# Optimization experiments

Hardware: AMD Instinct MI355X
Metric: run time of the kernel (lower is better)

## Reference

```python
import jax, jax.numpy as jnp
import numpy as np

N_NODES = 100000
N_EDGES = 3200000
F_IN = 128
NOUT = 32


def _lin(x, W, b):
    return x @ W + b


def _spect_conv(x, src, dst, W, b, n_nodes):
    # edge_attr is all-ones with a single frequency (K=1), so SpectConv reduces to
    # an unweighted scatter-add of linearly transformed source-node features.
    h = x @ W                                   # [N, nout]
    agg = jax.ops.segment_sum(h[src], dst, num_segments=n_nodes)  # [N, nout]
    return agg + b


def setup_inputs() -> dict:
    key = jax.random.key(0)
    ks = jax.random.split(key, 32)
    s = 0.05

    def w(k, shape):
        return jax.random.normal(k, shape, dtype=jnp.float32) * s

    inp = {
        "x": jax.random.normal(ks[0], (N_NODES, F_IN), dtype=jnp.float32),
        "edge_index": jax.random.randint(ks[1], (2, N_EDGES), 0, N_NODES, dtype=jnp.int32),
        # SpectConv weights (single frequency) + biases
        "Wc1": w(ks[2], (F_IN, NOUT)), "bc1": jnp.zeros((NOUT,), jnp.float32),
        "Wc2": w(ks[3], (NOUT, NOUT)), "bc2": jnp.zeros((NOUT,), jnp.float32),
        "Wc3": w(ks[4], (NOUT, NOUT)), "bc3": jnp.zeros((NOUT,), jnp.float32),
        # dense branch weights
        "W11": w(ks[5], (F_IN, NOUT)), "b11": w(ks[6], (NOUT,)),
        "W12": w(ks[7], (F_IN, NOUT)), "b12": w(ks[8], (NOUT,)),
        "W13": w(ks[9], (F_IN, NOUT)), "b13": w(ks[10], (NOUT,)),
        "W21": w(ks[11], (NOUT, NOUT)), "b21": w(ks[12], (NOUT,)),
        "W22": w(ks[13], (NOUT, NOUT)), "b22": w(ks[14], (NOUT,)),
        "W23": w(ks[15], (NOUT, NOUT)), "b23": w(ks[16], (NOUT,)),
        "W31": w(ks[17], (NOUT, NOUT)), "b31": w(ks[18], (NOUT,)),
        "W32": w(ks[19], (NOUT, NOUT)), "b32": w(ks[20], (NOUT,)),
        "W33": w(ks[21], (NOUT, NOUT)), "b33": w(ks[22], (NOUT,)),
        "W2": w(ks[23], (NOUT, 1)), "b2": w(ks[24], (1,)),
    }
    return inp


def reference(x, edge_index,
              Wc1, bc1, Wc2, bc2, Wc3, bc3,
              W11, b11, W12, b12, W13, b13,
              W21, b21, W22, b22, W23, b23,
              W31, b31, W32, b32, W33, b33,
              W2, b2):
    src, dst = edge_index[0], edge_index[1]
    n = x.shape[0]
    relu = jax.nn.relu

    def block(h, Wa, ba, Wc, bc, Wm1, bm1, Wm2, bm2):
        return (relu(_lin(h, Wa, ba))
                + relu(_spect_conv(h, src, dst, Wc, bc, n))
                + relu(_lin(h, Wm1, bm1) * _lin(h, Wm2, bm2)))

    h = block(x, W11, b11, Wc1, bc1, W12, b12, W13, b13)
    h = block(h, W21, b21, Wc2, bc2, W22, b22, W23, b23)
    h = block(h, W31, b31, Wc3, bc3, W32, b32, W33, b33)
    return _lin(h, W2, b2)
```

## Files before the change

kernel.cpp:

```cpp
#include <hip/hip_runtime.h>
#include <hip/hip_bf16.h>
#include <hip/hip_fp8.h>

#define N_FEAT 32
#define CBITS 7
#define CAP   6000
#define TILE  8192

typedef __attribute__((ext_vector_type(8))) short short8;
typedef __attribute__((ext_vector_type(4))) short short4e;
typedef __attribute__((ext_vector_type(4))) float floatx4;

static __device__ __forceinline__ unsigned short f2b(float f) {
    unsigned u = __float_as_uint(f);
    return (unsigned short)((u + 0x7FFFu + ((u >> 16) & 1u)) >> 16);
}
static __device__ __forceinline__ float b2f(unsigned short b) {
    return __uint_as_float(((unsigned)b) << 16);
}
static __device__ __forceinline__ unsigned char f2e(float f) {
    __hip_fp8_e4m3 v(f);
    return (unsigned char)v.__x;
}
static __device__ __forceinline__ float e2f(unsigned char b) {
    __hip_fp8_e4m3 v;
    v.__x = (__hip_fp8_storage_t)b;
    return (float)v;
}

template <int K, bool BF16_IN>
__global__ __launch_bounds__(256)
void transform_mfma_kernel(const void* __restrict__ hin,
                           const float* __restrict__ Wa, const float* __restrict__ ba,
                           const float* __restrict__ Wc,
                           const float* __restrict__ Wm1, const float* __restrict__ bm1,
                           const float* __restrict__ Wm2, const float* __restrict__ bm2,
                           unsigned short* __restrict__ t_pre, unsigned char* __restrict__ t_c,
                           int n_nodes)
{
    constexpr int WPITCH = (K == 32) ? 40 : 136;
    __shared__ unsigned short sW[128][WPITCH];

    const int t = threadIdx.x;
    const int node0 = blockIdx.x * 64;
    const int wave = t >> 6;
    const int lane = t & 63;
    const int m16 = lane & 15;
    const int quad = lane >> 4;

    for (int i = t; i < 128 * K; i += 256) {
        const int c = i & 127, kk = i >> 7;
        const int mat = c >> 5, cl = c & 31;
        const float* W = (mat == 0) ? Wa : (mat == 1) ? Wc : (mat == 2) ? Wm1 : Wm2;
        sW[c][kk] = f2b(W[(size_t)kk * 32 + cl]);
    }
    __syncthreads();

    const int n = node0 + wave * 16 + m16;
    const bool nok = (n < n_nodes);

    floatx4 acc[8];
#pragma unroll
    for (int i = 0; i < 8; ++i) acc[i] = (floatx4){0.f, 0.f, 0.f, 0.f};

#pragma unroll
    for (int k0 = 0; k0 < K; k0 += 32) {
        short8 a;
        if (BF16_IN) {
            const unsigned short* hb = (const unsigned short*)hin;
            a = nok ? *reinterpret_cast<const short8*>(hb + (size_t)n * K + k0 + quad * 8)
                    : (short8){0,0,0,0,0,0,0,0};
        } else {
            const float* hf = (const float*)hin;
            if (nok) {
                const floatx4 v0 = __builtin_nontemporal_load(
                    reinterpret_cast<const floatx4*>(hf + (size_t)n * K + k0 + quad * 8));
                const floatx4 v1 = __builtin_nontemporal_load(
                    reinterpret_cast<const floatx4*>(hf + (size_t)n * K + k0 + quad * 8 + 4));
                union { short8 v; unsigned short u[8]; } pk;
                pk.u[0] = f2b(v0[0]); pk.u[1] = f2b(v0[1]); pk.u[2] = f2b(v0[2]); pk.u[3] = f2b(v0[3]);
                pk.u[4] = f2b(v1[0]); pk.u[5] = f2b(v1[1]); pk.u[6] = f2b(v1[2]); pk.u[7] = f2b(v1[3]);
                a = pk.v;
            } else {
                a = (short8){0,0,0,0,0,0,0,0};
            }
        }
#pragma unroll
        for (int t8 = 0; t8 < 8; ++t8) {
            const short8 b = *reinterpret_cast<const short8*>(&sW[t8 * 16 + m16][k0 + quad * 8]);
            acc[t8] = __builtin_amdgcn_mfma_f32_16x16x32_bf16(a, b, acc[t8], 0, 0, 0);
        }
    }

#pragma unroll
    for (int r = 0; r < 4; ++r) {
        const int node = node0 + wave * 16 + quad * 4 + r;
        if (node < n_nodes) {
#pragma unroll
            for (int half = 0; half < 2; ++half) {
                const int c = m16 + half * 16;
                const float av  = acc[0 + half][r] + ba[c];
                const float wcv = acc[2 + half][r];
                const float m1  = acc[4 + half][r] + bm1[c];
                const float m2  = acc[6 + half][r] + bm2[c];
                t_pre[(size_t)node * N_FEAT + c] = f2b(fmaxf(av, 0.f) + fmaxf(m1 * m2, 0.f));
                t_c[(size_t)node * N_FEAT + c] = f2e(wcv);
            }
        }
    }
}

__global__ __launch_bounds__(1024)
void coarse_bin_kernel(const int* __restrict__ src, const int* __restrict__ dst,
                       unsigned* __restrict__ cnt_g, unsigned* __restrict__ binned,
                       int n_edges, int n_buckets)
{
    __shared__ unsigned sorted[TILE];
    __shared__ unsigned short buck[TILE];
    __shared__ unsigned hist[1024];
    __shared__ unsigned lbase[1024];
    __shared__ unsigned gofs[1024];
    __shared__ unsigned wsum[16], woff[16];

    const int t = threadIdx.x;
    const int wave = t >> 6, lane = t & 63;
    const int e0 = blockIdx.x * TILE;
    const int cnt = min(TILE, n_edges - e0);
    if (cnt <= 0) return;

    hist[t] = 0;
    __syncthreads();

    unsigned dv[TILE / 1024], sv[TILE / 1024];
    int nk = 0;
    for (int i = t; i < cnt; i += 1024, ++nk) {
        dv[nk] = (unsigned)dst[e0 + i];
        sv[nk] = (unsigned)src[e0 + i];
        atomicAdd(&hist[dv[nk] >> CBITS], 1u);
    }
    __syncthreads();

    const unsigned myh = hist[t];
    if (t < n_buckets)
        gofs[t] = myh ? atomicAdd(&cnt_g[t], myh) : 0u;

    unsigned v = myh;
#pragma unroll
    for (int off = 1; off < 64; off <<= 1) {
        const unsigned nv = __shfl_up(v, off);
        if (lane >= off) v += nv;
    }
    if (lane == 63) wsum[wave] = v;
    __syncthreads();
    if (t < 16) {
        unsigned s = wsum[t];
#pragma unroll
        for (int off = 1; off < 16; off <<= 1) {
            const unsigned nv = __shfl_up(s, off, 16);
            if (t >= off) s += nv;
        }
        woff[t] = s - wsum[t];
    }
    hist[t] = 0;
    __syncthreads();
    const unsigned lb_mine = v + woff[wave] - myh;
    lbase[t] = lb_mine;
    __syncthreads();

    for (int k = 0; k < nk; ++k) {
        const unsigned b = dv[k] >> CBITS;
        const unsigned pos = lbase[b] + atomicAdd(&hist[b], 1u);
        sorted[pos] = ((dv[k] & ((1u << CBITS) - 1)) << 17) | sv[k];
        buck[pos] = (unsigned short)b;
    }
    __syncthreads();

    for (int p = t; p < cnt; p += 1024) {
        const unsigned b = buck[p];
        const unsigned gp = gofs[b] + ((unsigned)p - lbase[b]);
        if (gp < CAP) binned[(size_t)b * CAP + gp] = sorted[p];
    }
}

__global__ __launch_bounds__(512)
void fine_sort_kernel(const unsigned* __restrict__ binned,
                      const unsigned* __restrict__ cnt_g,
                      unsigned* __restrict__ total_ctr,
                      int* __restrict__ srcs,
                      unsigned* __restrict__ rowstart, unsigned* __restrict__ rowend,
                      int n_nodes, int n_buckets)
{
    __shared__ int sorted_src[CAP];
    __shared__ unsigned hist[512];
    __shared__ unsigned incl[512];
    __shared__ unsigned ebase[512];
    __shared__ unsigned wsum[8], woff[8];
    __shared__ unsigned ob_s;

    const int t = threadIdx.x;
    const int wave = t >> 6, lane = t & 63;
    const int b = blockIdx.x;
    const unsigned cnt = min(cnt_g[b], (unsigned)CAP);
    const int node0 = b << CBITS;
    const int nodes_here = min(128, n_nodes - node0);
    const unsigned* tile = binned + (size_t)b * CAP;

    if (t == 0) ob_s = atomicAdd(total_ctr, cnt);
    hist[t] = 0;
    __syncthreads();
    const unsigned ob = ob_s;

    for (unsigned i = t; i < cnt; i += 512) {
        const unsigned e = tile[i];
        atomicAdd(&hist[((e >> 17) << 2) | ((e & 0x1FFFFu) >> 15)], 1u);
    }
    __syncthreads();

    const unsigned myh = hist[t];
    unsigned v = myh;
#pragma unroll
    for (int off = 1; off < 64; off <<= 1) {
        const unsigned nv = __shfl_up(v, off);
        if (lane >= off) v += nv;
    }
    if (lane == 63) wsum[wave] = v;
    __syncthreads();
    if (t < 8) {
        unsigned s = wsum[t];
#pragma unroll
        for (int off = 1; off < 8; off <<= 1) {
            const unsigned nv = __shfl_up(s, off, 8);
            if (t >= off) s += nv;
        }
        woff[t] = s - wsum[t];
    }
    hist[t] = 0;
    __syncthreads();
    const unsigned my_incl = v + woff[wave];
    incl[t] = my_incl;
    ebase[t] = my_incl - myh;
    __syncthreads();

    if (t < nodes_here) {
        rowstart[node0 + t] = ob + ebase[t << 2];
        rowend[node0 + t]   = ob + incl[(t << 2) + 3];
    }

    for (unsigned i = t; i < cnt; i += 512) {
        const unsigned e = tile[i];
        const unsigned key = ((e >> 17) << 2) | ((e & 0x1FFFFu) >> 15);
        const unsigned pos = ebase[key] + atomicAdd(&hist[key], 1u);
        sorted_src[pos] = (int)(e & 0x1FFFFu);
    }
    __syncthreads();
    for (unsigned i = t; i < cnt; i += 512)
        srcs[ob + i] = sorted_src[i];
}

static __device__ __forceinline__ void add4e(float* a, unsigned v) {
    a[0] += e2f((unsigned char)(v & 0xffu));
    a[1] += e2f((unsigned char)((v >> 8) & 0xffu));
    a[2] += e2f((unsigned char)((v >> 16) & 0xffu));
    a[3] += e2f((unsigned char)((v >> 24) & 0xffu));
}

__global__ __launch_bounds__(512)
void gather_transform_kernel(const unsigned char* __restrict__ t_c_in,
                             const unsigned short* __restrict__ t_pre_in,
                             const unsigned* __restrict__ rowstart,
                             const unsigned* __restrict__ rowend,
                             const int* __restrict__ srcs,
                             const float* __restrict__ bc,
                             const float* __restrict__ Wa, const float* __restrict__ ba,
                             const float* __restrict__ Wc,
                             const float* __restrict__ Wm1, const float* __restrict__ bm1,
                             const float* __restrict__ Wm2, const float* __restrict__ bm2,
                             unsigned short* __restrict__ t_pre_out,
                             unsigned char* __restrict__ t_c_out,
                             int n_nodes)
{
    __shared__ unsigned short sW[128][40];
    __shared__ unsigned short sH[64][40];

    const int t = threadIdx.x;
    const int node0 = blockIdx.x * 64;

    for (int i = t; i < 128 * 32; i += 512) {
        const int c = i & 127, kk = i >> 7;
        const int mat = c >> 5, cl = c & 31;
        const float* W = (mat == 0) ? Wa : (mat == 1) ? Wc : (mat == 2) ? Wm1 : Wm2;
        sW[c][kk] = f2b(W[(size_t)kk * 32 + cl]);
    }

    const int nl = t >> 3;
    const int node = node0 + nl;
    const int l8 = t & 7;
    const int f0 = l8 * 4;
    const bool nvalid = (node < n_nodes);

    if (nvalid) {
        const unsigned lo = rowstart[node], hi = rowend[node];
        float acc[4] = {0.f, 0.f, 0.f, 0.f};
        unsigned i = lo;

        if (i + 8 <= hi) {
            int sp[8];
#pragma unroll
            for (int j = 0; j < 8; ++j) sp[j] = srcs[i + j];
            for (;;) {
                unsigned v[8];
#pragma unroll
                for (int j = 0; j < 8; ++j)
                    v[j] = *reinterpret_cast<const unsigned*>(t_c_in + (size_t)sp[j] * N_FEAT + f0);
                i += 8;
                const bool more = (i + 8 <= hi);
                int sn[8];
#pragma unroll
                for (int j = 0; j < 8; ++j) {
                    const unsigned idx = more ? (i + j) : (hi - 1);
                    sn[j] = srcs[idx];
                }
#pragma unroll
                for (int j = 0; j < 8; ++j) add4e(acc, v[j]);
#pragma unroll
                for (int j = 0; j < 8; ++j) sp[j] = sn[j];
                if (!more) break;
            }
        }
        for (; i + 4 <= hi; i += 4) {
            unsigned v[4];
#pragma unroll
            for (int j = 0; j < 4; ++j)
                v[j] = *reinterpret_cast<const unsigned*>(
                    t_c_in + (size_t)srcs[i + j] * N_FEAT + f0);
#pragma unroll
            for (int j = 0; j < 4; ++j) add4e(acc, v[j]);
        }
        for (; i < hi; ++i)
            add4e(acc, *reinterpret_cast<const unsigned*>(
                t_c_in + (size_t)srcs[i] * N_FEAT + f0));

        const short4e p = *reinterpret_cast<const short4e*>(t_pre_in + (size_t)node * N_FEAT + f0);
        union { short4e v; unsigned short u[4]; } r;
#pragma unroll
        for (int j = 0; j < 4; ++j)
            r.u[j] = f2b(b2f((unsigned short)p[j]) + fmaxf(acc[j] + bc[f0 + j], 0.f));
        *reinterpret_cast<short4e*>(&sH[nl][f0]) = r.v;
    } else {
        *reinterpret_cast<short4e*>(&sH[nl][f0]) = (short4e){0, 0, 0, 0};
    }
    __syncthreads();

    const int wave = t >> 6;
    if (wave < 4) {
        const int lane = t & 63;
        const int m16 = lane & 15;
        const int quad = lane >> 4;

        floatx4 acc2[8];
#pragma unroll
        for (int i = 0; i < 8; ++i) acc2[i] = (floatx4){0.f, 0.f, 0.f, 0.f};

        const short8 a = *reinterpret_cast<const short8*>(&sH[wave * 16 + m16][quad * 8]);
#pragma unroll
        for (int t8 = 0; t8 < 8; ++t8) {
            const short8 b = *reinterpret_cast<const short8*>(&sW[t8 * 16 + m16][quad * 8]);
            acc2[t8] = __builtin_amdgcn_mfma_f32_16x16x32_bf16(a, b, acc2[t8], 0, 0, 0);
        }

#pragma unroll
        for (int r = 0; r < 4; ++r) {
            const int onode = node0 + wave * 16 + quad * 4 + r;
            if (onode < n_nodes) {
#pragma unroll
                for (int half = 0; half < 2; ++half) {
                    const int c = m16 + half * 16;
                    const float av  = acc2[0 + half][r] + ba[c];
                    const float wcv = acc2[2 + half][r];
                    const float m1  = acc2[4 + half][r] + bm1[c];
                    const float m2  = acc2[6 + half][r] + bm2[c];
                    t_pre_out[(size_t)onode * N_FEAT + c] = f2b(fmaxf(av, 0.f) + fmaxf(m1 * m2, 0.f));
                    t_c_out[(size_t)onode * N_FEAT + c] = f2e(wcv);
                }
            }
        }
    }
}

__global__ __launch_bounds__(256)
void gather_final_kernel(const unsigned char* __restrict__ t_c,
                         const unsigned short* __restrict__ t_pre,
                         const unsigned* __restrict__ rowstart,
                         const unsigned* __restrict__ rowend,
                         const int* __restrict__ srcs,
                         const float* __restrict__ bc, const float* __restrict__ W2,
                         const float* __restrict__ b2, float* __restrict__ out,
                         int n_nodes)
{
    const int node = blockIdx.x * 32 + (threadIdx.x >> 3);
    const int l8 = threadIdx.x & 7;
    const int f0 = l8 * 4;
    if (node >= n_nodes) return;
    const unsigned lo = rowstart[node], hi = rowend[node];
    float acc[4] = {0.f, 0.f, 0.f, 0.f};
    unsigned i = lo;

    if (i + 8 <= hi) {
        int sp[8];
#pragma unroll
        for (int j = 0; j < 8; ++j) sp[j] = srcs[i + j];
        for (;;) {
            unsigned v[8];
#pragma unroll
            for (int j = 0; j < 8; ++j)
                v[j] = *reinterpret_cast<const unsigned*>(t_c + (size_t)sp[j] * N_FEAT + f0);
            i += 8;
            const bool more = (i + 8 <= hi);
            int sn[8];
#pragma unroll
            for (int j = 0; j < 8; ++j) {
                const unsigned idx = more ? (i + j) : (hi - 1);
                sn[j] = srcs[idx];
            }
#pragma unroll
            for (int j = 0; j < 8; ++j) add4e(acc, v[j]);
#pragma unroll
            for (int j = 0; j < 8; ++j) sp[j] = sn[j];
            if (!more) break;
        }
    }
    for (; i + 4 <= hi; i += 4) {
        unsigned v[4];
#pragma unroll
        for (int j = 0; j < 4; ++j)
            v[j] = *reinterpret_cast<const unsigned*>(
                t_c + (size_t)srcs[i + j] * N_FEAT + f0);
#pragma unroll
        for (int j = 0; j < 4; ++j) add4e(acc, v[j]);
    }
    for (; i < hi; ++i)
        add4e(acc, *reinterpret_cast<const unsigned*>(
            t_c + (size_t)srcs[i] * N_FEAT + f0));

    const short4e p = *reinterpret_cast<const short4e*>(t_pre + (size_t)node * N_FEAT + f0);
    float r = 0.f;
#pragma unroll
    for (int j = 0; j < 4; ++j)
        r += (b2f((unsigned short)p[j]) + fmaxf(acc[j] + bc[f0 + j], 0.f)) * W2[f0 + j];
    r += __shfl_down(r, 4, 8);
    r += __shfl_down(r, 2, 8);
    r += __shfl_down(r, 1, 8);
    if (l8 == 0) out[node] = r + b2[0];
}

extern "C" void kernel_launch(void* const* d_in, const int* in_sizes, int n_in,
                              void* d_out, int out_size, void* d_ws, size_t ws_size,
                              hipStream_t stream)
{
    const float* x   = (const float*)d_in[0];
    const int*   ei  = (const int*)d_in[1];
    const float* Wc1 = (const float*)d_in[2];  const float* bc1 = (const float*)d_in[3];
    const float* Wc2 = (const float*)d_in[4];  const float* bc2 = (const float*)d_in[5];
    const float* Wc3 = (const float*)d_in[6];  const float* bc3 = (const float*)d_in[7];
    const float* W11 = (const float*)d_in[8];  const float* b11 = (const float*)d_in[9];
    const float* W12 = (const float*)d_in[10]; const float* b12 = (const float*)d_in[11];
    const float* W13 = (const float*)d_in[12]; const float* b13 = (const float*)d_in[13];
    const float* W21 = (const float*)d_in[14]; const float* b21 = (const float*)d_in[15];
    const float* W22 = (const float*)d_in[16]; const float* b22 = (const float*)d_in[17];
    const float* W23 = (const float*)d_in[18]; const float* b23 = (const float*)d_in[19];
    const float* W31 = (const float*)d_in[20]; const float* b31 = (const float*)d_in[21];
    const float* W32 = (const float*)d_in[22]; const float* b32 = (const float*)d_in[23];
    const float* W33 = (const float*)d_in[24]; const float* b33 = (const float*)d_in[25];
    const float* W2  = (const float*)d_in[26]; const float* b2  = (const float*)d_in[27];

    const int n_nodes = in_sizes[0] / 128;
    const int n_edges = in_sizes[1] / 2;
    const int* src = ei;
    const int* dst = ei + n_edges;
    const int n_buckets = (n_nodes + (1 << CBITS) - 1) >> CBITS;

    const size_t feat_elems = (size_t)n_nodes * N_FEAT;

    unsigned short* tpreA    = (unsigned short*)d_ws;
    unsigned short* tpreB    = tpreA + feat_elems;
    unsigned char*  tcA      = (unsigned char*)(tpreB + feat_elems);
    unsigned char*  tcB      = tcA + feat_elems;
    int*            srcs     = (int*)(tcB + feat_elems);
    unsigned*       rowstart = (unsigned*)(srcs + n_edges);
    unsigned*       rowend   = rowstart + n_nodes;
    unsigned*       cnt_g    = rowend + n_nodes;
    unsigned*       binned   = cnt_g + (n_buckets + 1);

    const int tf_grid = (n_nodes + 63) / 64;
    const int gt_grid = (n_nodes + 63) / 64;
    const int gf_grid = (n_nodes + 31) / 32;
    const int cb_grid = (n_edges + TILE - 1) / TILE;

    hipMemsetAsync(cnt_g, 0, ((size_t)n_buckets + 1) * sizeof(unsigned), stream);
    coarse_bin_kernel<<<cb_grid, 1024, 0, stream>>>(src, dst, cnt_g, binned, n_edges, n_buckets);
    fine_sort_kernel<<<n_buckets, 512, 0, stream>>>(
        binned, cnt_g, cnt_g + n_buckets, srcs, rowstart, rowend, n_nodes, n_buckets);

    transform_mfma_kernel<128, false><<<tf_grid, 256, 0, stream>>>(
        x, W11, b11, Wc1, W12, b12, W13, b13, tpreA, tcA, n_nodes);

    gather_transform_kernel<<<gt_grid, 512, 0, stream>>>(
        tcA, tpreA, rowstart, rowend, srcs, bc1,
        W21, b21, Wc2, W22, b22, W23, b23, tpreB, tcB, n_nodes);

    gather_transform_kernel<<<gt_grid, 512, 0, stream>>>(
        tcB, tpreB, rowstart, rowend, srcs, bc2,
        W31, b31, Wc3, W32, b32, W33, b33, tpreA, tcA, n_nodes);

    gather_final_kernel<<<gf_grid, 256, 0, stream>>>(
        tcA, tpreA, rowstart, rowend, srcs, bc3, W2, b2, (float*)d_out, n_nodes);
}
```

Measured before the change: 298.4 us.

## Fuse fine sort with first-layer transform and deepen gather prefetch to 16

Merges the per-bucket fine sort and the first-layer MFMA transform into a single launch. Block IDs below n_buckets do the sort and the rest do the transform on 128-node tiles with 512 threads, sharing one shared-memory buffer. The two independent workloads can now overlap on the GPU and one kernel launch is removed. Separately, the gather loops in both gather kernels prefetch 16 source indices per iteration instead of 8, which adds memory-level parallelism at the cost of more registers and a larger tail for short rows.

```diff
diff --git a/kernel.cpp b/kernel.cpp
--- a/kernel.cpp
+++ b/kernel.cpp
@@ -26,88 +26,6 @@
     __hip_fp8_e4m3 v;
     v.__x = (__hip_fp8_storage_t)b;
     return (float)v;
-}
-
-template <int K, bool BF16_IN>
-__global__ __launch_bounds__(256)
-void transform_mfma_kernel(const void* __restrict__ hin,
-                           const float* __restrict__ Wa, const float* __restrict__ ba,
-                           const float* __restrict__ Wc,
-                           const float* __restrict__ Wm1, const float* __restrict__ bm1,
-                           const float* __restrict__ Wm2, const float* __restrict__ bm2,
-                           unsigned short* __restrict__ t_pre, unsigned char* __restrict__ t_c,
-                           int n_nodes)
-{
-    constexpr int WPITCH = (K == 32) ? 40 : 136;
-    __shared__ unsigned short sW[128][WPITCH];
-
-    const int t = threadIdx.x;
-    const int node0 = blockIdx.x * 64;
-    const int wave = t >> 6;
-    const int lane = t & 63;
-    const int m16 = lane & 15;
-    const int quad = lane >> 4;
-
-    for (int i = t; i < 128 * K; i += 256) {
-        const int c = i & 127, kk = i >> 7;
-        const int mat = c >> 5, cl = c & 31;
-        const float* W = (mat == 0) ? Wa : (mat == 1) ? Wc : (mat == 2) ? Wm1 : Wm2;
-        sW[c][kk] = f2b(W[(size_t)kk * 32 + cl]);
-    }
-    __syncthreads();
-
-    const int n = node0 + wave * 16 + m16;
-    const bool nok = (n < n_nodes);
-
-    floatx4 acc[8];
-#pragma unroll
-    for (int i = 0; i < 8; ++i) acc[i] = (floatx4){0.f, 0.f, 0.f, 0.f};
-
-#pragma unroll
-    for (int k0 = 0; k0 < K; k0 += 32) {
-        short8 a;
-        if (BF16_IN) {
-            const unsigned short* hb = (const unsigned short*)hin;
-            a = nok ? *reinterpret_cast<const short8*>(hb + (size_t)n * K + k0 + quad * 8)
-                    : (short8){0,0,0,0,0,0,0,0};
-        } else {
-            const float* hf = (const float*)hin;
-            if (nok) {
-                const floatx4 v0 = __builtin_nontemporal_load(
-                    reinterpret_cast<const floatx4*>(hf + (size_t)n * K + k0 + quad * 8));
-                const floatx4 v1 = __builtin_nontemporal_load(
-                    reinterpret_cast<const floatx4*>(hf + (size_t)n * K + k0 + quad * 8 + 4));
-                union { short8 v; unsigned short u[8]; } pk;
-                pk.u[0] = f2b(v0[0]); pk.u[1] = f2b(v0[1]); pk.u[2] = f2b(v0[2]); pk.u[3] = f2b(v0[3]);
-                pk.u[4] = f2b(v1[0]); pk.u[5] = f2b(v1[1]); pk.u[6] = f2b(v1[2]); pk.u[7] = f2b(v1[3]);
-                a = pk.v;
-            } else {
-                a = (short8){0,0,0,0,0,0,0,0};
-            }
-        }
-#pragma unroll
-        for (int t8 = 0; t8 < 8; ++t8) {
-            const short8 b = *reinterpret_cast<const short8*>(&sW[t8 * 16 + m16][k0 + quad * 8]);
-            acc[t8] = __builtin_amdgcn_mfma_f32_16x16x32_bf16(a, b, acc[t8], 0, 0, 0);
-        }
-    }
-
-#pragma unroll
-    for (int r = 0; r < 4; ++r) {
-        const int node = node0 + wave * 16 + quad * 4 + r;
-        if (node < n_nodes) {
-#pragma unroll
-            for (int half = 0; half < 2; ++half) {
-                const int c = m16 + half * 16;
-                const float av  = acc[0 + half][r] + ba[c];
-                const float wcv = acc[2 + half][r];
-                const float m1  = acc[4 + half][r] + bm1[c];
-                const float m2  = acc[6 + half][r] + bm2[c];
-                t_pre[(size_t)node * N_FEAT + c] = f2b(fmaxf(av, 0.f) + fmaxf(m1 * m2, 0.f));
-                t_c[(size_t)node * N_FEAT + c] = f2e(wcv);
-            }
-        }
-    }
 }
 
 __global__ __launch_bounds__(1024)
@@ -183,78 +101,155 @@
 }
 
 __global__ __launch_bounds__(512)
-void fine_sort_kernel(const unsigned* __restrict__ binned,
-                      const unsigned* __restrict__ cnt_g,
-                      unsigned* __restrict__ total_ctr,
-                      int* __restrict__ srcs,
-                      unsigned* __restrict__ rowstart, unsigned* __restrict__ rowend,
-                      int n_nodes, int n_buckets)
+void fine_t1_fused_kernel(
+                          const unsigned* __restrict__ binned,
+                          const unsigned* __restrict__ cnt_g,
+                          unsigned* __restrict__ total_ctr,
+                          int* __restrict__ srcs,
+                          unsigned* __restrict__ rowstart, unsigned* __restrict__ rowend,
+                          int n_nodes, int n_buckets,
+                          const float* __restrict__ x,
+                          const float* __restrict__ Wa, const float* __restrict__ ba,
+                          const float* __restrict__ Wc,
+                          const float* __restrict__ Wm1, const float* __restrict__ bm1,
+                          const float* __restrict__ Wm2, const float* __restrict__ bm2,
+                          unsigned short* __restrict__ t_pre, unsigned char* __restrict__ t_c)
 {
-    __shared__ int sorted_src[CAP];
-    __shared__ unsigned hist[512];
-    __shared__ unsigned incl[512];
-    __shared__ unsigned ebase[512];
-    __shared__ unsigned wsum[8], woff[8];
-    __shared__ unsigned ob_s;
+    __shared__ __align__(16) unsigned char smem[34816];
 
     const int t = threadIdx.x;
-    const int wave = t >> 6, lane = t & 63;
-    const int b = blockIdx.x;
-    const unsigned cnt = min(cnt_g[b], (unsigned)CAP);
-    const int node0 = b << CBITS;
-    const int nodes_here = min(128, n_nodes - node0);
-    const unsigned* tile = binned + (size_t)b * CAP;
-
-    if (t == 0) ob_s = atomicAdd(total_ctr, cnt);
-    hist[t] = 0;
-    __syncthreads();
-    const unsigned ob = ob_s;
-
-    for (unsigned i = t; i < cnt; i += 512) {
-        const unsigned e = tile[i];
-        atomicAdd(&hist[((e >> 17) << 2) | ((e & 0x1FFFFu) >> 15)], 1u);
-    }
-    __syncthreads();
-
-    const unsigned myh = hist[t];
-    unsigned v = myh;
-#pragma unroll
-    for (int off = 1; off < 64; off <<= 1) {
-        const unsigned nv = __shfl_up(v, off);
-        if (lane >= off) v += nv;
-    }
-    if (lane == 63) wsum[wave] = v;
-    __syncthreads();
-    if (t < 8) {
-        unsigned s = wsum[t];
-#pragma unroll
-        for (int off = 1; off < 8; off <<= 1) {
-            const unsigned nv = __shfl_up(s, off, 8);
-            if (t >= off) s += nv;
-        }
-        woff[t] = s - wsum[t];
-    }
-    hist[t] = 0;
-    __syncthreads();
-    const unsigned my_incl = v + woff[wave];
-    incl[t] = my_incl;
-    ebase[t] = my_incl - myh;
-    __syncthreads();
-
-    if (t < nodes_here) {
-        rowstart[node0 + t] = ob + ebase[t << 2];
-        rowend[node0 + t]   = ob + incl[(t << 2) + 3];
-    }
-
-    for (unsigned i = t; i < cnt; i += 512) {
-        const unsigned e = tile[i];
-        const unsigned key = ((e >> 17) << 2) | ((e & 0x1FFFFu) >> 15);
-        const unsigned pos = ebase[key] + atomicAdd(&hist[key], 1u);
-        sorted_src[pos] = (int)(e & 0x1FFFFu);
-    }
-    __syncthreads();
-    for (unsigned i = t; i < cnt; i += 512)
-        srcs[ob + i] = sorted_src[i];
+
+    if ((int)blockIdx.x < n_buckets) {
+        int*      sorted_src = (int*)smem;
+        unsigned* hist       = (unsigned*)(smem + 24000);
+        unsigned* incl       = (unsigned*)(smem + 26048);
+        unsigned* ebase      = (unsigned*)(smem + 28096);
+        unsigned* wsum       = (unsigned*)(smem + 30144);
+        unsigned* woff       = (unsigned*)(smem + 30176);
+        unsigned* ob_s       = (unsigned*)(smem + 30208);
+
+        const int wave = t >> 6, lane = t & 63;
+        const int b = blockIdx.x;
+        const unsigned cnt = min(cnt_g[b], (unsigned)CAP);
+        const int node0 = b << CBITS;
+        const int nodes_here = min(128, n_nodes - node0);
+        const unsigned* tile = binned + (size_t)b * CAP;
+
+        if (t == 0) *ob_s = atomicAdd(total_ctr, cnt);
+        hist[t] = 0;
+        __syncthreads();
+        const unsigned ob = *ob_s;
+
+        for (unsigned i = t; i < cnt; i += 512) {
+            const unsigned e = tile[i];
+            atomicAdd(&hist[((e >> 17) << 2) | ((e & 0x1FFFFu) >> 15)], 1u);
+        }
+        __syncthreads();
+
+        const unsigned myh = hist[t];
+        unsigned v = myh;
+#pragma unroll
+        for (int off = 1; off < 64; off <<= 1) {
+            const unsigned nv = __shfl_up(v, off);
+            if (lane >= off) v += nv;
+        }
+        if (lane == 63) wsum[wave] = v;
+        __syncthreads();
+        if (t < 8) {
+            unsigned s = wsum[t];
+#pragma unroll
+            for (int off = 1; off < 8; off <<= 1) {
+                const unsigned nv = __shfl_up(s, off, 8);
+                if (t >= off) s += nv;
+            }
+            woff[t] = s - wsum[t];
+        }
+        hist[t] = 0;
+        __syncthreads();
+        const unsigned my_incl = v + woff[wave];
+        incl[t] = my_incl;
+        ebase[t] = my_incl - myh;
+        __syncthreads();
+
+        if (t < nodes_here) {
+            rowstart[node0 + t] = ob + ebase[t << 2];
+            rowend[node0 + t]   = ob + incl[(t << 2) + 3];
+        }
+
+        for (unsigned i = t; i < cnt; i += 512) {
+            const unsigned e = tile[i];
+            const unsigned key = ((e >> 17) << 2) | ((e & 0x1FFFFu) >> 15);
+            const unsigned pos = ebase[key] + atomicAdd(&hist[key], 1u);
+            sorted_src[pos] = (int)(e & 0x1FFFFu);
+        }
+        __syncthreads();
+        for (unsigned i = t; i < cnt; i += 512)
+            srcs[ob + i] = sorted_src[i];
+    } else {
+        typedef unsigned short (*sWt)[136];
+        sWt sW = (sWt)smem;
+
+        const int tb = blockIdx.x - n_buckets;
+        const int node0 = tb * 128;
+        const int wave = t >> 6;
+        const int lane = t & 63;
+        const int m16 = lane & 15;
+        const int quad = lane >> 4;
+
+        for (int i = t; i < 128 * 128; i += 512) {
+            const int c = i & 127, kk = i >> 7;
+            const int mat = c >> 5, cl = c & 31;
+            const float* W = (mat == 0) ? Wa : (mat == 1) ? Wc : (mat == 2) ? Wm1 : Wm2;
+            sW[c][kk] = f2b(W[(size_t)kk * 32 + cl]);
+        }
+        __syncthreads();
+
+        const int n = node0 + wave * 16 + m16;
+        const bool nok = (n < n_nodes);
+
+        floatx4 acc[8];
+#pragma unroll
+        for (int i = 0; i < 8; ++i) acc[i] = (floatx4){0.f, 0.f, 0.f, 0.f};
+
+#pragma unroll
+        for (int k0 = 0; k0 < 128; k0 += 32) {
+            short8 a;
+            if (nok) {
+                const floatx4 v0 = __builtin_nontemporal_load(
+                    reinterpret_cast<const floatx4*>(x + (size_t)n * 128 + k0 + quad * 8));
+                const floatx4 v1 = __builtin_nontemporal_load(
+                    reinterpret_cast<const floatx4*>(x + (size_t)n * 128 + k0 + quad * 8 + 4));
+                union { short8 v; unsigned short u[8]; } pk;
+                pk.u[0] = f2b(v0[0]); pk.u[1] = f2b(v0[1]); pk.u[2] = f2b(v0[2]); pk.u[3] = f2b(v0[3]);
+                pk.u[4] = f2b(v1[0]); pk.u[5] = f2b(v1[1]); pk.u[6] = f2b(v1[2]); pk.u[7] = f2b(v1[3]);
+                a = pk.v;
+            } else {
+                a = (short8){0,0,0,0,0,0,0,0};
+            }
+#pragma unroll
+            for (int t8 = 0; t8 < 8; ++t8) {
+                const short8 b = *reinterpret_cast<const short8*>(&sW[t8 * 16 + m16][k0 + quad * 8]);
+                acc[t8] = __builtin_amdgcn_mfma_f32_16x16x32_bf16(a, b, acc[t8], 0, 0, 0);
+            }
+        }
+
+#pragma unroll
+        for (int r = 0; r < 4; ++r) {
+            const int node = node0 + wave * 16 + quad * 4 + r;
+            if (node < n_nodes) {
+#pragma unroll
+                for (int half = 0; half < 2; ++half) {
+                    const int c = m16 + half * 16;
+                    const float av  = acc[0 + half][r] + ba[c];
+                    const float wcv = acc[2 + half][r];
+                    const float m1  = acc[4 + half][r] + bm1[c];
+                    const float m2  = acc[6 + half][r] + bm2[c];
+                    t_pre[(size_t)node * N_FEAT + c] = f2b(fmaxf(av, 0.f) + fmaxf(m1 * m2, 0.f));
+                    t_c[(size_t)node * N_FEAT + c] = f2e(wcv);
+                }
+            }
+        }
+    }
 }
 
 static __device__ __forceinline__ void add4e(float* a, unsigned v) {
@@ -303,27 +298,27 @@
         float acc[4] = {0.f, 0.f, 0.f, 0.f};
         unsigned i = lo;
 
-        if (i + 8 <= hi) {
-            int sp[8];
-#pragma unroll
-            for (int j = 0; j < 8; ++j) sp[j] = srcs[i + j];
+        if (i + 16 <= hi) {
+            int sp[16];
+#pragma unroll
+            for (int j = 0; j < 16; ++j) sp[j] = srcs[i + j];
             for (;;) {
-                unsigned v[8];
-#pragma unroll
-                for (int j = 0; j < 8; ++j)
+                unsigned v[16];
+#pragma unroll
+                for (int j = 0; j < 16; ++j)
                     v[j] = *reinterpret_cast<const unsigned*>(t_c_in + (size_t)sp[j] * N_FEAT + f0);
-                i += 8;
-                const bool more = (i + 8 <= hi);
-                int sn[8];
-#pragma unroll
-                for (int j = 0; j < 8; ++j) {
+                i += 16;
+                const bool more = (i + 16 <= hi);
+                int sn[16];
+#pragma unroll
+                for (int j = 0; j < 16; ++j) {
                     const unsigned idx = more ? (i + j) : (hi - 1);
                     sn[j] = srcs[idx];
                 }
 #pragma unroll
-                for (int j = 0; j < 8; ++j) add4e(acc, v[j]);
-#pragma unroll
-                for (int j = 0; j < 8; ++j) sp[j] = sn[j];
+                for (int j = 0; j < 16; ++j) add4e(acc, v[j]);
+#pragma unroll
+                for (int j = 0; j < 16; ++j) sp[j] = sn[j];
                 if (!more) break;
             }
         }
@@ -405,27 +400,27 @@
     float acc[4] = {0.f, 0.f, 0.f, 0.f};
     unsigned i = lo;
 
-    if (i + 8 <= hi) {
-        int sp[8];
-#pragma unroll
-        for (int j = 0; j < 8; ++j) sp[j] = srcs[i + j];
+    if (i + 16 <= hi) {
+        int sp[16];
+#pragma unroll
+        for (int j = 0; j < 16; ++j) sp[j] = srcs[i + j];
         for (;;) {
-            unsigned v[8];
-#pragma unroll
-            for (int j = 0; j < 8; ++j)
+            unsigned v[16];
+#pragma unroll
+            for (int j = 0; j < 16; ++j)
                 v[j] = *reinterpret_cast<const unsigned*>(t_c + (size_t)sp[j] * N_FEAT + f0);
-            i += 8;
-            const bool more = (i + 8 <= hi);
-            int sn[8];
-#pragma unroll
-            for (int j = 0; j < 8; ++j) {
+            i += 16;
+            const bool more = (i + 16 <= hi);
+            int sn[16];
+#pragma unroll
+            for (int j = 0; j < 16; ++j) {
                 const unsigned idx = more ? (i + j) : (hi - 1);
                 sn[j] = srcs[idx];
             }
 #pragma unroll
-            for (int j = 0; j < 8; ++j) add4e(acc, v[j]);
-#pragma unroll
-            for (int j = 0; j < 8; ++j) sp[j] = sn[j];
+            for (int j = 0; j < 16; ++j) add4e(acc, v[j]);
+#pragma unroll
+            for (int j = 0; j < 16; ++j) sp[j] = sn[j];
             if (!more) break;
         }
     }
@@ -491,18 +486,18 @@
     unsigned*       cnt_g    = rowend + n_nodes;
     unsigned*       binned   = cnt_g + (n_buckets + 1);
 
-    const int tf_grid = (n_nodes + 63) / 64;
+    const int t1_grid = (n_nodes + 127) / 128;
     const int gt_grid = (n_nodes + 63) / 64;
     const int gf_grid = (n_nodes + 31) / 32;
     const int cb_grid = (n_edges + TILE - 1) / TILE;
 
     hipMemsetAsync(cnt_g, 0, ((size_t)n_buckets + 1) * sizeof(unsigned), stream);
+
     coarse_bin_kernel<<<cb_grid, 1024, 0, stream>>>(src, dst, cnt_g, binned, n_edges, n_buckets);
-    fine_sort_kernel<<<n_buckets, 512, 0, stream>>>(
-        binned, cnt_g, cnt_g + n_buckets, srcs, rowstart, rowend, n_nodes, n_buckets);
-
-    transform_mfma_kernel<128, false><<<tf_grid, 256, 0, stream>>>(
-        x, W11, b11, Wc1, W12, b12, W13, b13, tpreA, tcA, n_nodes);
+
+    fine_t1_fused_kernel<<<n_buckets + t1_grid, 512, 0, stream>>>(
+        binned, cnt_g, cnt_g + n_buckets, srcs, rowstart, rowend, n_nodes, n_buckets,
+        x, W11, b11, Wc1, W12, b12, W13, b13, tpreA, tcA);
 
     gather_transform_kernel<<<gt_grid, 512, 0, stream>>>(
         tcA, tpreA, rowstart, rowend, srcs, bc1,
```

Result: no change. 299.9 us (+0.5%).
